# Kernel tuning notes

Hardware: AMD Instinct MI355X
Metric: run time of the kernel (lower is better)

## Reference

```python
import jax, jax.numpy as jnp
import numpy as np
from jax import lax

_T, _B, _I, _H = 2048, 1024, 15, 10


def setup_inputs() -> dict:
    key = jax.random.key(0)
    k1, k2, k3, k4, k5 = jax.random.split(key, 5)
    s = 1.0 / np.sqrt(_H)  # PyTorch LSTM init range
    return {
        "x": jax.random.normal(k1, (_T, _B, _I), dtype=jnp.float32),
        "h0": jax.random.normal(k2, (1, _B, _H), dtype=jnp.float32),
        "c0": jax.random.normal(k3, (1, _B, _H), dtype=jnp.float32),
        "W_ih": jax.random.uniform(k4, (4 * _H, _I), dtype=jnp.float32, minval=-s, maxval=s),
        "W_hh": jax.random.uniform(k5, (4 * _H, _H), dtype=jnp.float32, minval=-s, maxval=s),
    }


def _lstm(x, h0, c0, W_ih, W_hh):
    # Precompute input contribution for all timesteps: (T, B, 4H)
    pre = jnp.einsum('tbi,gi->tbg', x, W_ih)

    def step(carry, pre_t):
        h, c = carry  # (B, H) each
        gates = pre_t + h @ W_hh.T  # (B, 4H)
        i, f, g, o = jnp.split(gates, 4, axis=-1)  # PyTorch gate order i,f,g,o
        i = jax.nn.sigmoid(i)
        f = jax.nn.sigmoid(f)
        g = jnp.tanh(g)
        o = jax.nn.sigmoid(o)
        c = f * c + i * g
        h = o * jnp.tanh(c)
        return (h, c), h

    (hT, cT), out = lax.scan(step, (h0[0], c0[0]), pre)
    return out, hT[None, :, :], cT[None, :, :]


def reference(x, h0, c0, W_ih, W_hh):
    out, hN, cN = _lstm(x, h0, c0, W_ih, W_hh)
    return out, hN, cN
```

## Files before the change

### kernel.cpp

```cpp
#include <hip/hip_runtime.h>


#define T_N  2048
#define B_N  1024
#define I_N  15
#define H_N  10
#define DQ   32
#define NBLK (T_N / DQ)
#define LPAD 64

typedef _Float16 half2_t __attribute__((ext_vector_type(2)));
typedef _Float16 f16x8   __attribute__((ext_vector_type(8)));
typedef float    f32x16  __attribute__((ext_vector_type(16)));

template <int CTRL>
static __device__ __forceinline__ float dppf(float v) {
    return __builtin_bit_cast(float,
        __builtin_amdgcn_mov_dpp(__builtin_bit_cast(int, v), CTRL, 0xF, 0xF, true));
}
static __device__ __forceinline__ float rl(float v, int lane) {
    return __builtin_bit_cast(float, __builtin_amdgcn_readlane(__builtin_bit_cast(int, v), lane));
}
static __device__ __forceinline__ unsigned rlu(unsigned v, int lane) {
    return (unsigned)__builtin_amdgcn_readlane((int)v, lane);
}
static __device__ __forceinline__ half2_t h2(unsigned u) {
    return __builtin_bit_cast(half2_t, u);
}

#define BAR() asm volatile("s_waitcnt lgkmcnt(0)\n\ts_barrier" ::: "memory")

#define CSTEP(xav) do {                                                           \
    float A  = __builtin_amdgcn_fdot2(h2(hp0), wf0, (xav), false);                \
    A        = __builtin_amdgcn_fdot2(h2(hp1), wf1, A,     false);                \
    float Bv = __builtin_amdgcn_fdot2(h2(hp2), wf2, 0.f,   false);                \
    Bv       = __builtin_amdgcn_fdot2(h2(hp3), wf3, Bv,    false);                \
    const float Cv = __builtin_amdgcn_fdot2(h2(hp4), wf4, 0.f, false);            \
    const float acc = (A + Bv) + Cv;                                              \
    const float e   = __builtin_amdgcn_exp2f(acc);                                \
    const float rc  = __builtin_amdgcn_rcpf(1.0f + e);                            \
    const float act = fmaf(Aact, rc, Bact);                                       \
    const float iv  = dppf<0x00>(act);                                            \
    const float fv  = dppf<0x55>(act);                                            \
    const float gv  = dppf<0xAA>(act);                  \
    const float ov  = dppf<0xFF>(act);                                            \
    const float ovm2 = -2.0f * ov;                                 \
    cs = fmaf(fv, cs, iv * gv);                              \
    const float tt = __builtin_amdgcn_exp2f(cs);                                  \
    const float rr = __builtin_amdgcn_rcpf(1.0f + tt);                            \
    h = fmaf(ovm2, rr, ov);                                                       \
    const float hbv = dppf<0x104>(h);          \
    const unsigned pkh = __builtin_bit_cast(unsigned,                             \
                             __builtin_amdgcn_cvt_pkrtz(h, hbv));                 \
    hp0 = rlu(pkh, 0); hp1 = rlu(pkh, 8); hp2 = rlu(pkh, 16);                     \
    hp3 = rlu(pkh, 24); hp4 = rlu(pkh, 32);                                       \
} while (0)

#define CBLOCK(XC, XN, SLOTN, PAR) do {                                           \
    const float* nb = &buf[SLOTN][0][crow];                                       \
    _Pragma("unroll")                                                             \
    for (int d = 0; d < DQ; ++d) {                                                \
        CSTEP(XC[d]);                                                             \
        XN[d] = nb[d * LPAD];                                                     \
        hsh[PAR][d][lane] = h;                                                    \
    }                                                                             \
} while (0)

#define PLOADX(KB) do {                                                           \
    int t = (KB) * DQ + trow; if (t > T_N - 1) t = T_N - 1;                       \
    const float* xp = x + ((size_t)t * B_N + b) * I_N + koff;                     \
    _Pragma("unroll")                                                             \
    for (int e = 0; e < 8; ++e) xr[e] = (koff + e < I_N) ? xp[e] : 0.0f;          \
} while (0)

#define PPROJ(SLOT) do {                                                          \
    f16x8 af;                                                                     \
    _Pragma("unroll")                                                             \
    for (int e = 0; e < 8; ++e) af[e] = (_Float16)xr[e];                          \
    const f32x16 dA = __builtin_amdgcn_mfma_f32_32x32x16_f16(af, bf0, z16, 0, 0, 0); \
    const f32x16 dB = __builtin_amdgcn_mfma_f32_32x32x16_f16(af, bf1, z16, 0, 0, 0); \
    _Pragma("unroll")                                                             \
    for (int r = 0; r < 16; ++r) {                                                \
        const int rw = (r & 3) + 8 * (r >> 2) + rbase;                            \
        buf[SLOT][rw][ncol]      = dA[r];                                         \
        buf[SLOT][rw][ncol + 32] = dB[r];            \
    }                                                                             \
} while (0)

#define HSTORE(MB) do {                                                           \
    const int par_ = (MB) & 1;                                                    \
    if (sact) {                                                                   \
        _Pragma("unroll")                                                         \
        for (int r = 0; r < 6; ++r) {                                             \
            const int dd = r * 6 + sl_d;                                          \
            if (dd < DQ)                                                          \
                out[((size_t)(MB) * DQ + dd) * (B_N * H_N) + b * H_N + sl_j]      \
                    = hsh[par_][dd][4 * sl_j];                                    \
        }                                                                         \
    }                                                                             \
} while (0)

__global__ __launch_bounds__(128, 2)
void lstm_pc(const float* __restrict__ x, const float* __restrict__ h0,
             const float* __restrict__ c0, const float* __restrict__ Wih,
             const float* __restrict__ Whh, float* __restrict__ out)
{
    __shared__ float buf[3][DQ][LPAD];
    __shared__ float hsh[2][DQ][64];

    const int tid  = threadIdx.x;
    const int wave = tid >> 6;
    const int lane = tid & 63;
    const int b    = blockIdx.x;
    const float LOG2E = 1.4426950408889634f;

    const int trow  = lane & 31;
    const int koff  = (lane >> 5) * 8;
    const int ncol  = lane & 31;
    const int rbase = 4 * (lane >> 5);
    const int sl_j  = lane % H_N;
    const int sl_d  = lane / H_N;
    const bool sact = lane < 60;
    f16x8 bf0, bf1;
    f32x16 z16;
    float xr[8];

    const int p = lane & 3;
    int j = lane >> 2; if (j > H_N - 1) j = H_N - 1;
    const int crow = p * H_N + j;
    const bool writer = (wave == 0) && (p == 0) && (lane < 4 * H_N);
    const float Aact = (p == 2) ? -4.0f * LOG2E : 1.0f;
    const float Bact = (p == 2) ?  2.0f * LOG2E : 0.0f;
    half2_t wf0, wf1, wf2, wf3, wf4;
    float cs, h;
    unsigned hp0, hp1, hp2, hp3, hp4;
    float xqA[DQ], xqB[DQ];

    if (wave == 1) {
        __builtin_amdgcn_s_setprio(0);
#pragma unroll
        for (int e = 0; e < 8; ++e) {
            const int k = koff + e;
            {
                const int n = ncol;
                const float sgn = (n >= 20 && n < 30) ? 2.0f * LOG2E : -LOG2E;
                bf0[e] = (_Float16)((k < I_N) ? sgn * Wih[n * I_N + k] : 0.0f);
            }
            {
                const int n = 32 + ncol;
                const float sgn = (n >= 20 && n < 30) ? 2.0f * LOG2E : -LOG2E;
                bf1[e] = (_Float16)((k < I_N && n < 40) ? sgn * Wih[n * I_N + k] : 0.0f);
            }
        }
#pragma unroll
        for (int r = 0; r < 16; ++r) z16[r] = 0.0f;
        PLOADX(0);
        PPROJ(0);
        PLOADX(1);
        PPROJ(1);
        PLOADX(2);
    } else {
        __builtin_amdgcn_s_setprio(1);
        const float sg = (p == 2) ? 2.0f * LOG2E : -LOG2E;
        const float* wr = Whh + crow * H_N;
        half2_t w;
        w[0] = (_Float16)(sg * wr[0]); w[1] = (_Float16)(sg * wr[1]); wf0 = w;
        w[0] = (_Float16)(sg * wr[2]); w[1] = (_Float16)(sg * wr[3]); wf1 = w;
        w[0] = (_Float16)(sg * wr[4]); w[1] = (_Float16)(sg * wr[5]); wf2 = w;
        w[0] = (_Float16)(sg * wr[6]); w[1] = (_Float16)(sg * wr[7]); wf3 = w;
        w[0] = (_Float16)(sg * wr[8]); w[1] = (_Float16)(sg * wr[9]); wf4 = w;
        cs = c0[b * H_N + j] * (2.0f * LOG2E);
        h  = h0[b * H_N + j];
        const float hbv = dppf<0x104>(h);
        const unsigned pkh = __builtin_bit_cast(unsigned,
                                 __builtin_amdgcn_cvt_pkrtz(h, hbv));
        hp0 = rlu(pkh, 0); hp1 = rlu(pkh, 8); hp2 = rlu(pkh, 16);
        hp3 = rlu(pkh, 24); hp4 = rlu(pkh, 32);
    }
    BAR();

    if (wave == 0) {
#pragma unroll
        for (int d = 0; d < DQ; ++d) xqA[d] = buf[0][d][crow];
    }

    int slR = 1, slW = 2, slO = 0;
    for (int m = 0; m < NBLK; m += 2) {
        if (wave == 1) {
            PPROJ(slW);
            PLOADX(m + 3);
            if (m > 0) HSTORE(m - 1);
        } else {
            CBLOCK(xqA, xqB, slR, 0);
        }
        BAR();
        { const int t = slO; slO = slR; slR = slW; slW = t; }
        if (wave == 1) {
            PPROJ(slW);
            PLOADX(m + 4);
            HSTORE(m);
        } else {
            CBLOCK(xqB, xqA, slR, 1);
        }
        BAR();
        { const int t = slO; slO = slR; slR = slW; slW = t; }
    }

    if (wave == 1) {
        HSTORE(NBLK - 1);
    } else if (writer) {
        const size_t base = (size_t)T_N * B_N * H_N;
        out[base + b * H_N + j] = h;
        out[base + (size_t)B_N * H_N + b * H_N + j] = cs * 0.34657359027997264f;
    }
}

extern "C" void kernel_launch(void* const* d_in, const int* in_sizes, int n_in,
                              void* d_out, int out_size, void* d_ws, size_t ws_size,
                              hipStream_t stream) {
    const float* x   = (const float*)d_in[0];
    const float* h0  = (const float*)d_in[1];
    const float* c0  = (const float*)d_in[2];
    const float* Wih = (const float*)d_in[3];
    const float* Whh = (const float*)d_in[4];
    float* out = (float*)d_out;
    lstm_pc<<<dim3(B_N), dim3(128), 0, stream>>>(x, h0, c0, Wih, Whh, out);
}
```

Baseline: 182.2 us.

## Replace fp16 packed dot recurrence with fp32 FMAs and scalar readlane broadcasts

The recurrent h·W_hh product now uses ten fp32 FMAs with fp32 weights and hidden values, instead of five fp16 fdot2 ops on packed half2 values. The h broadcast uses ten readlanes, replacing the DPP shuffle, fp16 pack and five readlanes. The gate activation fma is restructured so only the g lane computes the tanh transform before its DPP. The hsh row is also padded to 65 to change LDS bank mapping. This removes the conversion and packing from the serial dependency chain and improves accuracy, but adds more readlane and FMA instructions per step.

```diff
diff --git a/kernel.cpp b/kernel.cpp
--- a/kernel.cpp
+++ b/kernel.cpp
@@ -8,8 +8,8 @@
 #define DQ   32
 #define NBLK (T_N / DQ)
 #define LPAD 64
-
-typedef _Float16 half2_t __attribute__((ext_vector_type(2)));
+#define HPAD 65
+
 typedef _Float16 f16x8   __attribute__((ext_vector_type(8)));
 typedef float    f32x16  __attribute__((ext_vector_type(16)));
 
@@ -21,39 +21,32 @@
 static __device__ __forceinline__ float rl(float v, int lane) {
     return __builtin_bit_cast(float, __builtin_amdgcn_readlane(__builtin_bit_cast(int, v), lane));
 }
-static __device__ __forceinline__ unsigned rlu(unsigned v, int lane) {
-    return (unsigned)__builtin_amdgcn_readlane((int)v, lane);
-}
-static __device__ __forceinline__ half2_t h2(unsigned u) {
-    return __builtin_bit_cast(half2_t, u);
-}
 
 #define BAR() asm volatile("s_waitcnt lgkmcnt(0)\n\ts_barrier" ::: "memory")
 
 #define CSTEP(xav) do {                                                           \
-    float A  = __builtin_amdgcn_fdot2(h2(hp0), wf0, (xav), false);                \
-    A        = __builtin_amdgcn_fdot2(h2(hp1), wf1, A,     false);                \
-    float Bv = __builtin_amdgcn_fdot2(h2(hp2), wf2, 0.f,   false);                \
-    Bv       = __builtin_amdgcn_fdot2(h2(hp3), wf3, Bv,    false);                \
-    const float Cv = __builtin_amdgcn_fdot2(h2(hp4), wf4, 0.f, false);            \
-    const float acc = (A + Bv) + Cv;                                              \
+    float d0 = fmaf(hs0, wh0, (xav)); d0 = fmaf(hs5, wh5, d0);                    \
+    float d1 = hs1 * wh1;             d1 = fmaf(hs6, wh6, d1);                    \
+    float d2 = hs2 * wh2;             d2 = fmaf(hs7, wh7, d2);                    \
+    float d3 = hs3 * wh3;             d3 = fmaf(hs8, wh8, d3);                    \
+    float d4 = hs4 * wh4;             d4 = fmaf(hs9, wh9, d4);                    \
+    const float acc = (d0 + d1 + d2) + (d3 + d4);                                 \
     const float e   = __builtin_amdgcn_exp2f(acc);                                \
     const float rc  = __builtin_amdgcn_rcpf(1.0f + e);                            \
-    const float act = fmaf(Aact, rc, Bact);                                       \
-    const float iv  = dppf<0x00>(act);                                            \
-    const float fv  = dppf<0x55>(act);                                            \
-    const float gv  = dppf<0xAA>(act);                  \
-    const float ov  = dppf<0xFF>(act);                                            \
-    const float ovm2 = -2.0f * ov;                                 \
-    cs = fmaf(fv, cs, iv * gv);                              \
+    const float iv  = dppf<0x00>(rc);                     \
+    const float fv  = dppf<0x55>(rc);                                             \
+    const float ov  = dppf<0xFF>(rc);                                             \
+    const float g2  = fmaf(-5.7707801635558534f, rc, 2.8853900817779267f);        \
+    const float gv  = dppf<0xAA>(g2);             \
+    const float fvcs = fv * cs;                                                   \
+    cs = fmaf(gv, iv, fvcs);                                 \
     const float tt = __builtin_amdgcn_exp2f(cs);                                  \
     const float rr = __builtin_amdgcn_rcpf(1.0f + tt);                            \
+    const float ovm2 = -2.0f * ov;                                 \
     h = fmaf(ovm2, rr, ov);                                                       \
-    const float hbv = dppf<0x104>(h);          \
-    const unsigned pkh = __builtin_bit_cast(unsigned,                             \
-                             __builtin_amdgcn_cvt_pkrtz(h, hbv));                 \
-    hp0 = rlu(pkh, 0); hp1 = rlu(pkh, 8); hp2 = rlu(pkh, 16);                     \
-    hp3 = rlu(pkh, 24); hp4 = rlu(pkh, 32);                                       \
+    hs0 = rl(h, 0);  hs1 = rl(h, 4);  hs2 = rl(h, 8);  hs3 = rl(h, 12);           \
+    hs4 = rl(h, 16); hs5 = rl(h, 20); hs6 = rl(h, 24); hs7 = rl(h, 28);           \
+    hs8 = rl(h, 32); hs9 = rl(h, 36);                                             \
 } while (0)
 
 #define CBLOCK(XC, XN, SLOTN, PAR) do {                                           \
@@ -106,7 +99,7 @@
              const float* __restrict__ Whh, float* __restrict__ out)
 {
     __shared__ float buf[3][DQ][LPAD];
-    __shared__ float hsh[2][DQ][64];
+    __shared__ float hsh[2][DQ][HPAD];
 
     const int tid  = threadIdx.x;
     const int wave = tid >> 6;
@@ -129,11 +122,9 @@
     int j = lane >> 2; if (j > H_N - 1) j = H_N - 1;
     const int crow = p * H_N + j;
     const bool writer = (wave == 0) && (p == 0) && (lane < 4 * H_N);
-    const float Aact = (p == 2) ? -4.0f * LOG2E : 1.0f;
-    const float Bact = (p == 2) ?  2.0f * LOG2E : 0.0f;
-    half2_t wf0, wf1, wf2, wf3, wf4;
+    float wh0, wh1, wh2, wh3, wh4, wh5, wh6, wh7, wh8, wh9;
     float cs, h;
-    unsigned hp0, hp1, hp2, hp3, hp4;
+    float hs0, hs1, hs2, hs3, hs4, hs5, hs6, hs7, hs8, hs9;
     float xqA[DQ], xqB[DQ];
 
     if (wave == 1) {
@@ -163,19 +154,14 @@
         __builtin_amdgcn_s_setprio(1);
         const float sg = (p == 2) ? 2.0f * LOG2E : -LOG2E;
         const float* wr = Whh + crow * H_N;
-        half2_t w;
-        w[0] = (_Float16)(sg * wr[0]); w[1] = (_Float16)(sg * wr[1]); wf0 = w;
-        w[0] = (_Float16)(sg * wr[2]); w[1] = (_Float16)(sg * wr[3]); wf1 = w;
-        w[0] = (_Float16)(sg * wr[4]); w[1] = (_Float16)(sg * wr[5]); wf2 = w;
-        w[0] = (_Float16)(sg * wr[6]); w[1] = (_Float16)(sg * wr[7]); wf3 = w;
-        w[0] = (_Float16)(sg * wr[8]); w[1] = (_Float16)(sg * wr[9]); wf4 = w;
+        wh0 = sg * wr[0]; wh1 = sg * wr[1]; wh2 = sg * wr[2]; wh3 = sg * wr[3];
+        wh4 = sg * wr[4]; wh5 = sg * wr[5]; wh6 = sg * wr[6]; wh7 = sg * wr[7];
+        wh8 = sg * wr[8]; wh9 = sg * wr[9];
         cs = c0[b * H_N + j] * (2.0f * LOG2E);
         h  = h0[b * H_N + j];
-        const float hbv = dppf<0x104>(h);
-        const unsigned pkh = __builtin_bit_cast(unsigned,
-                                 __builtin_amdgcn_cvt_pkrtz(h, hbv));
-        hp0 = rlu(pkh, 0); hp1 = rlu(pkh, 8); hp2 = rlu(pkh, 16);
-        hp3 = rlu(pkh, 24); hp4 = rlu(pkh, 32);
+        hs0 = rl(h, 0);  hs1 = rl(h, 4);  hs2 = rl(h, 8);  hs3 = rl(h, 12);
+        hs4 = rl(h, 16); hs5 = rl(h, 20); hs6 = rl(h, 24); hs7 = rl(h, 28);
+        hs8 = rl(h, 32); hs9 = rl(h, 36);
     }
     BAR();
 
```

After: 409.0 us. 124% more time.
